# Performance work log

Measured on AMD Instinct MI355X. Metric: run time of the kernel, lower is better.

The kernel has to match this reference:

```python
import jax, jax.numpy as jnp
import numpy as np

SR = 44100.0
J, Q = 12, 16
W0 = 2.0 * np.pi      # MorletWavelet.freq_to_w_at_s(1.0, s=1.0) -> w = 2*pi*f*s
N_SIG = 3.0           # wavelet support = +/- N_SIG standard deviations


def _make_wavelet_bank():
    """Morlet filter bank: J octaves, Q steps/octave, highest freq = nyquist.
    Returns centered, zero-padded real/imag filter stacks of shape (K, Lmax)."""
    dt = 1.0 / SR
    nyq = SR / 2.0
    wavelets = []
    for j in range(J):
        for q in range(Q):
            f = nyq / (2.0 ** (j + q / Q))
            s = 1.0 / f                      # center freq f = W0/(2*pi*s) = 1/s
            M = int(np.ceil(N_SIG * s * SR))  # half support in samples
            t = np.arange(-M, M + 1) * dt
            psi = (np.pi ** -0.25) / np.sqrt(s) \
                * np.exp(1j * W0 * t / s) * np.exp(-0.5 * (t / s) ** 2)
            psi = psi / np.sum(np.abs(psi))   # L1 normalization
            wavelets.append(psi.astype(np.complex64))
    Lmax = max(len(p) for p in wavelets)       # odd (2*M_max + 1)
    bank = np.zeros((len(wavelets), Lmax), np.complex64)
    for i, p in enumerate(wavelets):
        left = (Lmax - len(p)) // 2            # center-pad each wavelet
        bank[i, left:left + len(p)] = p
    return bank


def setup_inputs() -> dict:
    key = jax.random.key(0)
    x = jax.random.normal(key, (2, 1, 32768), dtype=jnp.float32)
    bank = _make_wavelet_bank()
    return {
        "x": x,
        "filt_real": jnp.asarray(bank.real, dtype=jnp.float32),
        "filt_imag": jnp.asarray(bank.imag, dtype=jnp.float32),
    }


def _scat1d(x, filt_real, filt_imag):
    # x: (B, 1, T); filters: (K, L) with L odd. Equivalent to the torch path:
    # pad input by L//2, cross-correlate (F.conv1d) with each complex wavelet,
    # take the modulus. Done via FFT (same math, efficient for ~47k-tap kernels).
    K, L = filt_real.shape
    B, C, T = x.shape  # C == 1 (squeeze_channels=True)
    P = L // 2
    xp = jnp.pad(x[:, 0, :], ((0, 0), (P, P)))       # (B, T + 2P)
    n_full = xp.shape[-1] + L - 1
    N = 1 << (n_full - 1).bit_length()               # next pow2 FFT size
    X = jnp.fft.rfft(xp, N)                          # (B, N//2+1)
    Gr = jnp.fft.rfft(filt_real[:, ::-1], N)         # flip -> corr via conv
    Gi = jnp.fft.rfft(filt_imag[:, ::-1], N)         # (K, N//2+1)
    lo = L - 1                                       # valid-corr offset
    yr = jnp.fft.irfft(X[:, None, :] * Gr[None], N)[..., lo:lo + T]
    yi = jnp.fft.irfft(X[:, None, :] * Gi[None], N)[..., lo:lo + T]
    return jnp.sqrt(yr * yr + yi * yi)               # (B, K, T) modulus


def reference(x, filt_real, filt_imag):
    return _scat1d(x, filt_real, filt_imag)
```

## Files before the change

kernel.cpp:

```cpp
#include <hip/hip_runtime.h>
#include <math.h>

#define T_LEN   32768
#define NK      192
#define NB      2
#define KDIR    48
#define MAXM    56

struct SParams {
  int m1e[144];
  int slot[144];
  int voff[144];
  int ab[9];
  int jb[11];
};

__device__ __forceinline__ int j2_of_q(int q) {
  return 4 + (q >= 5) + (q >= 10) + (q >= 15);
}

__global__ __launch_bounds__(256) void k_pre(float* __restrict__ ws, SParams P,
                                             int zbase, int zn) {
  int tid = threadIdx.x;
  if (blockIdx.y == 144) {
    int stride = gridDim.x * 256;
    for (int i = blockIdx.x * 256 + tid; i < zn; i += stride) ws[zbase + i] = 0.f;
    return;
  }
  int ki = blockIdx.y;
  int slotc = P.slot[ki];
  int M1e = P.m1e[ki];
  float* dst = ws + P.voff[ki];
  int nent = 2 * M1e + 2;
  int k = ki + 48;
  int j = k >> 4, q = k & 15;
  float sig = 2.f * exp2f((float)(16 * j + q) * 0.0625f);
  float s1 = sig * 0.86602540378f;
  float gc = -0.5f / (s1 * s1);
  float om = 6.28318530718f / sig;
  float norm = 1.f / (2.50662827463f * s1 * erff((float)M1e / (1.41421356237f * s1)));
  #pragma unroll
  for (int e0 = 0; e0 < 4; ++e0) {
    int e = blockIdx.x * 1024 + e0 * 256 + tid;
    if (e >= slotc) continue;
    if (e >= nent) { dst[2 * e] = 0.f; dst[2 * e + 1] = 0.f; continue; }
    float mm = (float)(e - M1e);
    float g = __expf(gc * mm * mm) * norm;
    float sn, cs; __sincosf(om * mm, &sn, &cs);
    dst[2 * e] = g * cs;
    dst[2 * e + 1] = g * sn;
  }
}


template<int J, int G, int S, int CH>
__device__ __forceinline__ void deep_path(const float* __restrict__ x,
                                          float* __restrict__ ws, const SParams& P,
                                          int q, int rc, int tid,
                                          float* xs, float* red) {
  constexpr int d = 1 << J;
  constexpr int E = 2048;
  const int tile = rc / CH;
  const int chunk = rc % CH;
  const int ki = 16 * (J - 3) + q;
  const int J2 = j2_of_q(q);
  const int slot = P.slot[ki];
  const int e_base = chunk * (S * E);
  if (e_base >= slot) return;
  const int M1e = P.m1e[ki];
  const float* vt = ws + P.voff[ki];
  const int n0 = tile * G;
  const int ubase0 = (n0 - J2) * d - M1e;
  const float* xb0 = x;
  const float* xb1 = x + T_LEN;

  float acc[4 * G];
  #pragma unroll
  for (int i = 0; i < 4 * G; ++i) acc[i] = 0.f;

  #pragma unroll
  for (int s = 0; s < S; ++s) {
    int e0 = e_base + s * E;
    if (e0 >= slot) break;
    int Ech = slot - e0; if (Ech > E) Ech = E;
    int ub = ubase0 + e0;
    int Wn = Ech + (G - 1) * d + 2;
    if (ub < T_LEN && ub + Wn > 0) {
      int Wh = (Wn + 1) >> 1;
      for (int i = tid; i < Wh; i += 256) {
        int u0 = ub + 2 * i;
        bool ok = (unsigned)u0 <= (unsigned)(T_LEN - 2);
        int uc = ok ? u0 : 0;
        float2 a = *(const float2*)(xb0 + uc);
        float2 b = *(const float2*)(xb1 + uc);
        float4 w;
        w.x = ok ? a.x : 0.f; w.y = ok ? b.x : 0.f;
        w.z = ok ? a.y : 0.f; w.w = ok ? b.y : 0.f;
        *(float4*)(xs + 4 * i) = w;
      }
      __syncthreads();
      int pend = Ech >> 9;
      const float4* xp0 = (const float4*)xs + tid;
      const float* vte = vt + 2 * e0 + 4 * tid;
      float4 vp = *(const float4*)(vte);
      for (int ps = 0; ps < pend; ++ps) {
        float4 v = vp;
        if (ps + 1 < pend) vp = *(const float4*)(vte + ((ps + 1) << 10));
        const float4* xp = xp0 + (ps << 8);
        #pragma unroll
        for (int g = 0; g < G; ++g) {
          float4 xv = xp[g * (d >> 1)];
          acc[4 * g + 0] += v.x * xv.x + v.z * xv.z;
          acc[4 * g + 1] += v.y * xv.x + v.w * xv.z;
          acc[4 * g + 2] += v.x * xv.y + v.z * xv.w;
          acc[4 * g + 3] += v.y * xv.y + v.w * xv.w;
        }
      }
      __syncthreads();
    }
  }

  #pragma unroll
  for (int st = 1; st < 64; st <<= 1) {
    #pragma unroll
    for (int i = 0; i < 4 * G; ++i) acc[i] += __shfl_xor(acc[i], st, 64);
  }
  int wv = tid >> 6;
  if ((tid & 63) == 0) {
    #pragma unroll
    for (int gg = 0; gg < G; ++gg)
      *(float4*)(red + wv * 64 + 4 * gg) =
        make_float4(acc[4 * gg], acc[4 * gg + 1], acc[4 * gg + 2], acc[4 * gg + 3]);
  }
  __syncthreads();
  if (tid < 4 * G)
    red[256 + tid] = red[tid] + red[64 + tid] + red[128 + tid] + red[192 + tid];
  __syncthreads();
  if (tid < G) {
    int nidx = n0 + tid;
    int Ncu = (32767 >> J) + 17;
    if (nidx < Ncu) {
      float ar0 = red[256 + 4 * tid], ai0 = red[256 + 4 * tid + 1];
      float ar1 = red[256 + 4 * tid + 2], ai1 = red[256 + 4 * tid + 3];
      float ndf = (float)((nidx - J2) * d);
      float rev = ndf * exp2f(-(float)(16 * (J + 1) + q) * 0.0625f);
      rev -= floorf(rev);
      float sn, cs; __sincosf(rev * 6.28318530718f, &sn, &cs);
      float* ap = ws + P.ab[J - 3] + (q * 2) * Ncu * 2;
      float r0 = ar0 * cs - ai0 * sn, i0 = ar0 * sn + ai0 * cs;
      float r1 = ar1 * cs - ai1 * sn, i1 = ar1 * sn + ai1 * cs;
      if (CH == 1) {
        *(float2*)(ap + 2 * nidx) = make_float2(r0, i0);
        *(float2*)(ap + 2 * (Ncu + nidx)) = make_float2(r1, i1);
      } else {
        atomicAdd(ap + 2 * nidx, r0);
        atomicAdd(ap + 2 * nidx + 1, i0);
        atomicAdd(ap + 2 * (Ncu + nidx), r1);
        atomicAdd(ap + 2 * (Ncu + nidx) + 1, i1);
      }
    }
  }
}

template<int J, int TOUT, int LT>
__device__ __forceinline__ void small_path(const float* __restrict__ x,
                                           float* __restrict__ ws, const SParams& P,
                                           int q, int tile, int tid,
                                           float* xs, float* red) {
  constexpr int d = 1 << J;
  constexpr int TASKS = TOUT * 2;
  constexpr int SPLIT = 256 / TASKS;
  const int ki = 16 * (J - 3) + q;
  const int J2 = j2_of_q(q);
  const int M1e = P.m1e[ki];
  const int nent = 2 * M1e + 2;
  const float* vt = ws + P.voff[ki];
  const int Ncu = (32767 >> J) + 17;
  const int o0 = tile * TOUT;
  const int ub = (o0 - J2) * d - M1e;
  const int W = (TOUT - 1) * d + nent;
  const int PS = W + (((W - 1) >> J) << 1) + 4;
  const float* xb0 = x;
  const float* xb1 = x + T_LEN;
  for (int i = tid; i < W; i += 256) {
    int u = ub + i;
    bool ok = (unsigned)u < (unsigned)T_LEN;
    int uc = ok ? u : 0;
    float a = xb0[uc]; a = ok ? a : 0.f;
    float bv = xb1[uc]; bv = ok ? bv : 0.f;
    int ad = i + ((i >> J) << 1);
    xs[ad] = a; xs[PS + ad] = bv;
  }
  __syncthreads();
  int o = tid & (TOUT - 1);
  int b = (tid >> LT) & 1;
  int seg = tid >> (LT + 1);
  int per = ((nent >> 1) + SPLIT - 1) / SPLIT;
  int e_lo = 2 * per * seg; if (e_lo > nent) e_lo = nent;
  int e_hi = e_lo + 2 * per; if (e_hi > nent) e_hi = nent;
  const float* pl = xs + b * PS;
  int sb = o * d;
  float ar = 0.f, ai = 0.f;
  #pragma unroll 4
  for (int e = e_lo; e < e_hi; e += 2) {
    float4 v = *(const float4*)(vt + 2 * e);
    int s = sb + e;
    float2 xv = *(const float2*)(pl + s + ((s >> J) << 1));
    ar += v.x * xv.x + v.z * xv.y;
    ai += v.y * xv.x + v.w * xv.y;
  }
  if (SPLIT > 1) {
    red[tid] = ar; red[256 + tid] = ai;
    __syncthreads();
    if (seg == 0) {
      #pragma unroll
      for (int ss = 1; ss < SPLIT; ++ss) {
        ar += red[tid + ss * TASKS];
        ai += red[256 + tid + ss * TASKS];
      }
    }
  }
  if (seg == 0 && o0 + o < Ncu) {
    int nidx = o0 + o;
    float ndf = (float)((nidx - J2) * d);
    float rev = ndf * exp2f(-(float)(16 * (J + 1) + q) * 0.0625f);
    rev -= floorf(rev);
    float sn, cs; __sincosf(rev * 6.28318530718f, &sn, &cs);
    float* ap = ws + P.ab[J - 3] + (q * 2) * Ncu * 2;
    *(float2*)(ap + 2 * (b * Ncu + nidx)) = make_float2(ar * cs - ai * sn, ar * sn + ai * cs);
  }
}

__device__ __forceinline__ void direct_path(const float* __restrict__ x,
                                            const float* __restrict__ fr,
                                            const float* __restrict__ fi,
                                            float* __restrict__ out, int Lmax,
                                            int rem, int tid,
                                            float* xs, float* red) {
  int b = rem / 1536;
  int r2 = rem - b * 1536;
  int k = r2 >> 5;
  int t0 = (r2 & 31) << 10;
  int j = k >> 4, q = k & 15;
  int M = (int)ceil(6.0 * exp2((double)j + (double)q * 0.0625)) + 2;
  int P = Lmax >> 1;
  float* frs = red;
  float* fis = red + 128;
  int xlen = 1024 + 2 * M;
  const float* xb = x + b * T_LEN;
  for (int i = tid; i < xlen; i += 256) {
    int u = t0 - M + i;
    xs[i] = (u >= 0 && u < T_LEN) ? xb[u] : 0.f;
  }
  if (tid < 4) xs[xlen + tid] = 0.f;
  const float* frk = fr + (size_t)k * Lmax + (P - M);
  const float* fik = fi + (size_t)k * Lmax + (P - M);
  int tl = 2 * M + 1;
  for (int i = tid; i < tl; i += 256) { frs[i] = frk[i]; fis[i] = fik[i]; }
  if (tid < 3) { frs[tl + tid] = 0.f; fis[tl + tid] = 0.f; }
  __syncthreads();
  float ar0 = 0.f, ar1 = 0.f, ar2 = 0.f, ar3 = 0.f;
  float ai0 = 0.f, ai1 = 0.f, ai2 = 0.f, ai3 = 0.f;
  const float4* xsv = (const float4*)(xs + 4 * tid);
  float4 w0 = xsv[0];
  int groups = (tl + 3) >> 2;
  for (int g = 0; g < groups; ++g) {
    float4 w1 = xsv[g + 1];
    float4 f4 = *(const float4*)(frs + 4 * g);
    float4 h4 = *(const float4*)(fis + 4 * g);
    ar0 += f4.x * w0.x + f4.y * w0.y + f4.z * w0.z + f4.w * w0.w;
    ai0 += h4.x * w0.x + h4.y * w0.y + h4.z * w0.z + h4.w * w0.w;
    ar1 += f4.x * w0.y + f4.y * w0.z + f4.z * w0.w + f4.w * w1.x;
    ai1 += h4.x * w0.y + h4.y * w0.z + h4.z * w0.w + h4.w * w1.x;
    ar2 += f4.x * w0.z + f4.y * w0.w + f4.z * w1.x + f4.w * w1.y;
    ai2 += h4.x * w0.z + h4.y * w0.w + h4.z * w1.x + h4.w * w1.y;
    ar3 += f4.x * w0.w + f4.y * w1.x + f4.z * w1.y + f4.w * w1.z;
    ai3 += h4.x * w0.w + h4.y * w1.x + h4.z * w1.y + h4.w * w1.z;
    w0 = w1;
  }
  size_t ob = (size_t)(b * NK + k) * T_LEN + t0 + 4 * tid;
  float4 res;
  res.x = sqrtf(ar0 * ar0 + ai0 * ai0);
  res.y = sqrtf(ar1 * ar1 + ai1 * ai1);
  res.z = sqrtf(ar2 * ar2 + ai2 * ai2);
  res.w = sqrtf(ar3 * ar3 + ai3 * ai3);
  *(float4*)(out + ob) = res;
}

__global__ __launch_bounds__(256) void k_s1(const float* __restrict__ x,
                                            const float* __restrict__ fr,
                                            const float* __restrict__ fi,
                                            float* __restrict__ out, int Lmax,
                                            float* __restrict__ ws, SParams P) {
  __shared__ __align__(16) float xs[8200];
  __shared__ __align__(16) float red[512];
  int bx = blockIdx.x, tid = threadIdx.x;
  int o = 0;
  #pragma unroll
  for (int t = 1; t < 10; ++t) if (bx >= P.jb[t]) o = t;
  int rem = bx - P.jb[o];
  if (o == 9) { direct_path(x, fr, fi, out, Lmax, rem, tid, xs, red); return; }
  int j = 11 - o;
  int rc = rem >> 4, q = rem & 15;
  switch (j) {
    case 11: deep_path<11, 2, 3, 8>(x, ws, P, q, rc, tid, xs, red); break;
    case 10: deep_path<10, 3, 3, 4>(x, ws, P, q, rc, tid, xs, red); break;
    case 9:  deep_path<9, 4, 3, 2>(x, ws, P, q, rc, tid, xs, red); break;
    case 8:  deep_path<8, 8, 3, 1>(x, ws, P, q, rc, tid, xs, red); break;
    case 7:  deep_path<7, 16, 2, 1>(x, ws, P, q, rc, tid, xs, red); break;
    case 6:  small_path<6, 32, 5>(x, ws, P, q, rc, tid, xs, red); break;
    case 5:  small_path<5, 64, 6>(x, ws, P, q, rc, tid, xs, red); break;
    case 4:  small_path<4, 128, 7>(x, ws, P, q, rc, tid, xs, red); break;
    default: small_path<3, 128, 7>(x, ws, P, q, rc, tid, xs, red); break;
  }
}

__global__ __launch_bounds__(256) void k_stage2(const float* __restrict__ ws,
                                                float* __restrict__ out, SParams P) {
  __shared__ __align__(16) float sA[2][8][48][2];
  int by = blockIdx.y;
  int bx = blockIdx.x, tid = threadIdx.x;
  int k0 = KDIR + 2 * by;
  int j = k0 >> 4;
  int d = 1 << j;
  int Ncu = (32767 >> j) + 17;
  int nbb = (bx << 8) >> j;
  int sstep = 8192 >> j;
  #pragma unroll
  for (int kk = 0; kk < 2; ++kk) {
    int q = (k0 + kk) & 15;
    int ntap = 2 * j2_of_q(q) + 1;
    const float* A0 = ws + P.ab[j - 3] + (q * 2) * Ncu * 2;
    int Ci = (255 >> j) + ntap + 1;
    #pragma unroll
    for (int pi = 0; pi < 8; ++pi) {
      int i = pi & 3, p = pi >> 2;
      const float* Ap = A0 + p * Ncu * 2 + 2 * (nbb + i * sstep);
      for (int c = tid; c < Ci; c += 256)
        *(float2*)(&sA[kk][pi][c][0]) = *(const float2*)(Ap + 2 * c);
    }
  }
  __syncthreads();
  int t0 = (bx << 8) + tid;
  int phi = t0 & (d - 1);
  int nl = (t0 >> j) - nbb;
  float fd = (float)d;
  #pragma unroll
  for (int kk = 0; kk < 2; ++kk) {
    int k = k0 + kk, q = k & 15;
    int J2 = j2_of_q(q);
    int ntap = 2 * J2 + 1;
    float sig = 2.f * exp2f((float)(16 * j + q) * 0.0625f);
    float s2 = sig * 0.5f;
    float inv2 = 1.f / (s2 * s2);
    float u0 = (float)(phi + J2 * d);
    float eg = __expf(-0.5f * u0 * u0 * inv2);
    float mf = __expf((fd * u0 - 0.5f * fd * fd) * inv2);
    float qf = __expf(-fd * fd * inv2);
    float Z = 0.f;
    float sr0 = 0.f, si0 = 0.f, sr1 = 0.f, si1 = 0.f;
    float sr2 = 0.f, si2 = 0.f, sr3 = 0.f, si3 = 0.f;
    float tr0 = 0.f, ti0 = 0.f, tr1 = 0.f, ti1 = 0.f;
    float tr2 = 0.f, ti2 = 0.f, tr3 = 0.f, ti3 = 0.f;
    const float* base = &sA[kk][0][nl][0];
    for (int rr = 0; rr < ntap; ++rr) {
      float w = eg; eg *= mf; mf *= qf; Z += w;
      float2 a0 = *(const float2*)(base + (0 * 48 + rr) * 2);
      float2 a1 = *(const float2*)(base + (1 * 48 + rr) * 2);
      float2 a2 = *(const float2*)(base + (2 * 48 + rr) * 2);
      float2 a3 = *(const float2*)(base + (3 * 48 + rr) * 2);
      float2 b0 = *(const float2*)(base + (4 * 48 + rr) * 2);
      float2 b1 = *(const float2*)(base + (5 * 48 + rr) * 2);
      float2 b2 = *(const float2*)(base + (6 * 48 + rr) * 2);
      float2 b3 = *(const float2*)(base + (7 * 48 + rr) * 2);
      sr0 += w * a0.x; si0 += w * a0.y; sr1 += w * a1.x; si1 += w * a1.y;
      sr2 += w * a2.x; si2 += w * a2.y; sr3 += w * a3.x; si3 += w * a3.y;
      tr0 += w * b0.x; ti0 += w * b0.y; tr1 += w * b1.x; ti1 += w * b1.y;
      tr2 += w * b2.x; ti2 += w * b2.y; tr3 += w * b3.x; ti3 += w * b3.y;
    }
    float zi = 1.f / Z;
    size_t ob0 = (size_t)k * T_LEN + t0;
    size_t ob1 = (size_t)(NK + k) * T_LEN + t0;
    out[ob0]         = sqrtf(sr0 * sr0 + si0 * si0) * zi;
    out[ob0 + 8192]  = sqrtf(sr1 * sr1 + si1 * si1) * zi;
    out[ob0 + 16384] = sqrtf(sr2 * sr2 + si2 * si2) * zi;
    out[ob0 + 24576] = sqrtf(sr3 * sr3 + si3 * si3) * zi;
    out[ob1]         = sqrtf(tr0 * tr0 + ti0 * ti0) * zi;
    out[ob1 + 8192]  = sqrtf(tr1 * tr1 + ti1 * ti1) * zi;
    out[ob1 + 16384] = sqrtf(tr2 * tr2 + ti2 * ti2) * zi;
    out[ob1 + 24576] = sqrtf(tr3 * tr3 + ti3 * ti3) * zi;
  }
}

extern "C" void kernel_launch(void* const* d_in, const int* in_sizes, int n_in,
                              void* d_out, int out_size, void* d_ws, size_t ws_size,
                              hipStream_t stream) {
  const float* x  = (const float*)d_in[0];
  const float* fr = (const float*)d_in[1];
  const float* fi = (const float*)d_in[2];
  float* out = (float*)d_out;
  float* ws  = (float*)d_ws;
  int Lmax = in_sizes[1] / NK;

  SParams Pm;
  int cur = 0, maxslot = 0;
  for (int ki = 0; ki < 144; ++ki) {
    int j = (ki + 48) >> 4, q = ki & 15;
    double sig = 2.0 * exp2(((double)(16 * j + q)) / 16.0);
    double s1 = sig * 0.86602540378443864676;
    int M1 = (int)ceil(3.5 * s1);
    int M1e = (M1 + 1) & ~1;
    int slotc = (2 * M1e + 2 + 511) & ~511;
    Pm.m1e[ki] = M1e;
    Pm.slot[ki] = slotc;
    Pm.voff[ki] = cur;
    cur += 2 * slotc;
    if (slotc > maxslot) maxslot = slotc;
  }
  for (int j = 3; j <= 11; ++j) {
    Pm.ab[j - 3] = cur;
    cur += 32 * ((32767 >> j) + 17) * 2;
  }
  const int DG[5]  = {2, 3, 4, 8, 16};
  const int DCH[5] = {8, 4, 2, 1, 1};
  const int STO[4] = {32, 64, 128, 128};
  Pm.jb[0] = 0;
  for (int o = 0; o < 9; ++o) {
    int j = 11 - o;
    int Ncu = (32767 >> j) + 17;
    int cnt;
    if (o < 5) {
      int tiles = (Ncu + DG[o] - 1) / DG[o];
      cnt = tiles * DCH[o] * 16;
    } else {
      int TOUT = STO[o - 5];
      cnt = ((Ncu + TOUT - 1) / TOUT) * 16;
    }
    Pm.jb[o + 1] = Pm.jb[o] + cnt;
  }
  Pm.jb[10] = Pm.jb[9] + (T_LEN / 1024) * KDIR * NB;

  int zbase = Pm.ab[6];
  int zn = (Pm.ab[8] + 32 * ((32767 >> 11) + 17) * 2) - zbase;

  k_pre<<<dim3((maxslot + 1023) / 1024, 145), dim3(256), 0, stream>>>(ws, Pm, zbase, zn);
  k_s1<<<dim3(Pm.jb[10]), dim3(256), 0, stream>>>(x, fr, fi, out, Lmax, ws, Pm);
  k_stage2<<<dim3(T_LEN / (256 * 4), (NK - KDIR) / 2), dim3(256), 0, stream>>>(ws, out, Pm);
}
```

Before: 229.9 us.

## Add register-only path for deepest octaves and retune tile sizes

Adds a reg_path for octaves 11 and 10. It reads input samples straight from global memory into registers, without staging them in LDS, and splits the wavelet taps across chunks that merge their results through atomics. The deep_path tap chunk size E is made a template parameter and lowered, and the small_path output tile sizes are halved for octaves 4 to 6. Shared memory drops accordingly, which aims to raise occupancy and spread work over more blocks. The cost is more global traffic in the register path and more blocks and atomics overall.

```diff
diff --git a/kernel.cpp b/kernel.cpp
--- a/kernel.cpp
+++ b/kernel.cpp
@@ -53,13 +53,111 @@
 }
 
 
-template<int J, int G, int S, int CH>
+template<int J, int G, int CH>
+__device__ __forceinline__ void reg_path(const float* __restrict__ x,
+                                         float* __restrict__ ws, const SParams& P,
+                                         int q, int rc, int tid, float* red) {
+  constexpr int d = 1 << J;
+  const int tile = rc / CH;
+  const int chunk = rc % CH;
+  const int ki = 16 * (J - 3) + q;
+  const int J2 = j2_of_q(q);
+  const int slot = P.slot[ki];
+  const int per = ((slot + CH - 1) / CH + 511) & ~511;
+  const int c0 = chunk * per;
+  if (c0 >= slot) return;
+  int c1 = c0 + per; if (c1 > slot) c1 = slot;
+  const int M1e = P.m1e[ki];
+  const float* vt = ws + P.voff[ki];
+  const int n0 = tile * G;
+  const int ub0 = (n0 - J2) * d - M1e + c0;
+  const float* xb0 = x;
+  const float* xb1 = x + T_LEN;
+
+  float acc[4 * G];
+  #pragma unroll
+  for (int i = 0; i < 4 * G; ++i) acc[i] = 0.f;
+
+  int npass = (c1 - c0) >> 9;
+  const float* vte = vt + 2 * c0 + 4 * tid;
+  const int hi_lim = T_LEN - 512 - (G - 1) * d;
+  float4 vp = *(const float4*)vte;
+  for (int p = 0; p < npass; ++p) {
+    float4 v = vp;
+    if (p + 1 < npass) vp = *(const float4*)(vte + ((p + 1) << 10));
+    int ub = ub0 + (p << 9);
+    int u = ub + 2 * tid;
+    if (ub >= 0 && ub <= hi_lim) {
+      #pragma unroll
+      for (int g = 0; g < G; ++g) {
+        float2 a = *(const float2*)(xb0 + u + g * d);
+        float2 b = *(const float2*)(xb1 + u + g * d);
+        acc[4 * g + 0] += v.x * a.x + v.z * a.y;
+        acc[4 * g + 1] += v.y * a.x + v.w * a.y;
+        acc[4 * g + 2] += v.x * b.x + v.z * b.y;
+        acc[4 * g + 3] += v.y * b.x + v.w * b.y;
+      }
+    } else if (ub < T_LEN && ub + 512 + (G - 1) * d > 0) {
+      #pragma unroll
+      for (int g = 0; g < G; ++g) {
+        int ug = u + g * d;
+        int uc = min(max(ug, 0), T_LEN - 2);
+        float2 a = *(const float2*)(xb0 + uc);
+        float2 b = *(const float2*)(xb1 + uc);
+        bool ok = (unsigned)ug <= (unsigned)(T_LEN - 2);
+        float ax = ok ? a.x : 0.f, ay = ok ? a.y : 0.f;
+        float bx = ok ? b.x : 0.f, by = ok ? b.y : 0.f;
+        acc[4 * g + 0] += v.x * ax + v.z * ay;
+        acc[4 * g + 1] += v.y * ax + v.w * ay;
+        acc[4 * g + 2] += v.x * bx + v.z * by;
+        acc[4 * g + 3] += v.y * bx + v.w * by;
+      }
+    }
+  }
+
+  #pragma unroll
+  for (int st = 1; st < 64; st <<= 1) {
+    #pragma unroll
+    for (int i = 0; i < 4 * G; ++i) acc[i] += __shfl_xor(acc[i], st, 64);
+  }
+  int wv = tid >> 6;
+  if ((tid & 63) == 0) {
+    #pragma unroll
+    for (int gg = 0; gg < G; ++gg)
+      *(float4*)(red + wv * 64 + 4 * gg) =
+        make_float4(acc[4 * gg], acc[4 * gg + 1], acc[4 * gg + 2], acc[4 * gg + 3]);
+  }
+  __syncthreads();
+  if (tid < 4 * G)
+    red[256 + tid] = red[tid] + red[64 + tid] + red[128 + tid] + red[192 + tid];
+  __syncthreads();
+  if (tid < G) {
+    int nidx = n0 + tid;
+    int Ncu = (32767 >> J) + 17;
+    if (nidx < Ncu) {
+      float ar0 = red[256 + 4 * tid], ai0 = red[256 + 4 * tid + 1];
+      float ar1 = red[256 + 4 * tid + 2], ai1 = red[256 + 4 * tid + 3];
+      float ndf = (float)((nidx - J2) * d);
+      float rev = ndf * exp2f(-(float)(16 * (J + 1) + q) * 0.0625f);
+      rev -= floorf(rev);
+      float sn, cs; __sincosf(rev * 6.28318530718f, &sn, &cs);
+      float* ap = ws + P.ab[J - 3] + (q * 2) * Ncu * 2;
+      float r0 = ar0 * cs - ai0 * sn, i0 = ar0 * sn + ai0 * cs;
+      float r1 = ar1 * cs - ai1 * sn, i1 = ar1 * sn + ai1 * cs;
+      atomicAdd(ap + 2 * nidx, r0);
+      atomicAdd(ap + 2 * nidx + 1, i0);
+      atomicAdd(ap + 2 * (Ncu + nidx), r1);
+      atomicAdd(ap + 2 * (Ncu + nidx) + 1, i1);
+    }
+  }
+}
+
+template<int J, int G, int S, int CH, int E>
 __device__ __forceinline__ void deep_path(const float* __restrict__ x,
                                           float* __restrict__ ws, const SParams& P,
                                           int q, int rc, int tid,
                                           float* xs, float* red) {
   constexpr int d = 1 << J;
-  constexpr int E = 2048;
   const int tile = rc / CH;
   const int chunk = rc % CH;
   const int ki = 16 * (J - 3) + q;
@@ -292,7 +390,7 @@
                                             const float* __restrict__ fi,
                                             float* __restrict__ out, int Lmax,
                                             float* __restrict__ ws, SParams P) {
-  __shared__ __align__(16) float xs[8200];
+  __shared__ __align__(16) float xs[6920];
   __shared__ __align__(16) float red[512];
   int bx = blockIdx.x, tid = threadIdx.x;
   int o = 0;
@@ -303,14 +401,14 @@
   int j = 11 - o;
   int rc = rem >> 4, q = rem & 15;
   switch (j) {
-    case 11: deep_path<11, 2, 3, 8>(x, ws, P, q, rc, tid, xs, red); break;
-    case 10: deep_path<10, 3, 3, 4>(x, ws, P, q, rc, tid, xs, red); break;
-    case 9:  deep_path<9, 4, 3, 2>(x, ws, P, q, rc, tid, xs, red); break;
-    case 8:  deep_path<8, 8, 3, 1>(x, ws, P, q, rc, tid, xs, red); break;
-    case 7:  deep_path<7, 16, 2, 1>(x, ws, P, q, rc, tid, xs, red); break;
-    case 6:  small_path<6, 32, 5>(x, ws, P, q, rc, tid, xs, red); break;
-    case 5:  small_path<5, 64, 6>(x, ws, P, q, rc, tid, xs, red); break;
-    case 4:  small_path<4, 128, 7>(x, ws, P, q, rc, tid, xs, red); break;
+    case 11: reg_path<11, 2, 8>(x, ws, P, q, rc, tid, red); break;
+    case 10: reg_path<10, 3, 4>(x, ws, P, q, rc, tid, red); break;
+    case 9:  deep_path<9, 4, 4, 2, 1536>(x, ws, P, q, rc, tid, xs, red); break;
+    case 8:  deep_path<8, 8, 4, 1, 1536>(x, ws, P, q, rc, tid, xs, red); break;
+    case 7:  deep_path<7, 16, 2, 1, 1536>(x, ws, P, q, rc, tid, xs, red); break;
+    case 6:  small_path<6, 16, 4>(x, ws, P, q, rc, tid, xs, red); break;
+    case 5:  small_path<5, 32, 5>(x, ws, P, q, rc, tid, xs, red); break;
+    case 4:  small_path<4, 64, 6>(x, ws, P, q, rc, tid, xs, red); break;
     default: small_path<3, 128, 7>(x, ws, P, q, rc, tid, xs, red); break;
   }
 }
@@ -423,7 +521,7 @@
   }
   const int DG[5]  = {2, 3, 4, 8, 16};
   const int DCH[5] = {8, 4, 2, 1, 1};
-  const int STO[4] = {32, 64, 128, 128};
+  const int STO[4] = {16, 32, 64, 128};
   Pm.jb[0] = 0;
   for (int o = 0; o < 9; ++o) {
     int j = 11 - o;
```

New measurement: 227.4 us. No clear change (-1.1%).

## Stream deep-octave correlation from a zero-padded input in registers

Applied to the files above, without the earlier changes.

A pre-pass now writes a zero-padded copy of both input batches into the workspace, so every path can read the signal without bounds checks. The shared-memory-staged deep path is replaced by a register path that reads the padded input and filter taps straight from global memory. It uses double-buffered loads, a fixed group of 4 outputs, and chunked reduction. The small-path tile sizes are reduced and shared memory halved with a launch-bounds occupancy hint of 8, trading more blocks and global cache traffic for fewer syncs and higher occupancy.

```diff
diff --git a/kernel.cpp b/kernel.cpp
--- a/kernel.cpp
+++ b/kernel.cpp
@@ -6,6 +6,9 @@
 #define NB      2
 #define KDIR    48
 #define MAXM    56
+#define PADL    40960
+#define PADR    40960
+#define XLEN    (PADL + T_LEN + PADR)
 
 struct SParams {
   int m1e[144];
@@ -13,15 +16,27 @@
   int voff[144];
   int ab[9];
   int jb[11];
+  int xoff;
 };
 
 __device__ __forceinline__ int j2_of_q(int q) {
   return 4 + (q >= 5) + (q >= 10) + (q >= 15);
 }
 
-__global__ __launch_bounds__(256) void k_pre(float* __restrict__ ws, SParams P,
+__global__ __launch_bounds__(256) void k_pre(const float* __restrict__ x,
+                                             float* __restrict__ ws, SParams P,
                                              int zbase, int zn) {
   int tid = threadIdx.x;
+  if (blockIdx.y == 145) {
+    int stride = gridDim.x * 256;
+    float* xp = ws + P.xoff;
+    for (int i = blockIdx.x * 256 + tid; i < 2 * XLEN; i += stride) {
+      int b = i >= XLEN;
+      int u = i - (b ? XLEN : 0) - PADL;
+      xp[i] = ((unsigned)u < (unsigned)T_LEN) ? x[b * T_LEN + u] : 0.f;
+    }
+    return;
+  }
   if (blockIdx.y == 144) {
     int stride = gridDim.x * 256;
     for (int i = blockIdx.x * 256 + tid; i < zn; i += stride) ws[zbase + i] = 0.f;
@@ -53,95 +68,102 @@
 }
 
 
-template<int J, int G, int S, int CH>
-__device__ __forceinline__ void deep_path(const float* __restrict__ x,
-                                          float* __restrict__ ws, const SParams& P,
-                                          int q, int rc, int tid,
-                                          float* xs, float* red) {
+template<int J, int CH>
+__device__ __forceinline__ void reg_path(const float* __restrict__ xpad,
+                                         float* __restrict__ ws, const SParams& P,
+                                         int q, int rc, int tid, float* red) {
   constexpr int d = 1 << J;
-  constexpr int E = 2048;
   const int tile = rc / CH;
   const int chunk = rc % CH;
   const int ki = 16 * (J - 3) + q;
   const int J2 = j2_of_q(q);
   const int slot = P.slot[ki];
-  const int e_base = chunk * (S * E);
-  if (e_base >= slot) return;
+  const int per = CH == 1 ? slot : (((slot + CH - 1) / CH + 511) & ~511);
+  const int c0 = chunk * per;
+  if (c0 >= slot) return;
+  int c1 = c0 + per; if (c1 > slot) c1 = slot;
   const int M1e = P.m1e[ki];
   const float* vt = ws + P.voff[ki];
-  const int n0 = tile * G;
-  const int ubase0 = (n0 - J2) * d - M1e;
-  const float* xb0 = x;
-  const float* xb1 = x + T_LEN;
-
-  float acc[4 * G];
-  #pragma unroll
-  for (int i = 0; i < 4 * G; ++i) acc[i] = 0.f;
-
-  #pragma unroll
-  for (int s = 0; s < S; ++s) {
-    int e0 = e_base + s * E;
-    if (e0 >= slot) break;
-    int Ech = slot - e0; if (Ech > E) Ech = E;
-    int ub = ubase0 + e0;
-    int Wn = Ech + (G - 1) * d + 2;
-    if (ub < T_LEN && ub + Wn > 0) {
-      int Wh = (Wn + 1) >> 1;
-      for (int i = tid; i < Wh; i += 256) {
-        int u0 = ub + 2 * i;
-        bool ok = (unsigned)u0 <= (unsigned)(T_LEN - 2);
-        int uc = ok ? u0 : 0;
-        float2 a = *(const float2*)(xb0 + uc);
-        float2 b = *(const float2*)(xb1 + uc);
-        float4 w;
-        w.x = ok ? a.x : 0.f; w.y = ok ? b.x : 0.f;
-        w.z = ok ? a.y : 0.f; w.w = ok ? b.y : 0.f;
-        *(float4*)(xs + 4 * i) = w;
-      }
-      __syncthreads();
-      int pend = Ech >> 9;
-      const float4* xp0 = (const float4*)xs + tid;
-      const float* vte = vt + 2 * e0 + 4 * tid;
-      float4 vp = *(const float4*)(vte);
-      for (int ps = 0; ps < pend; ++ps) {
-        float4 v = vp;
-        if (ps + 1 < pend) vp = *(const float4*)(vte + ((ps + 1) << 10));
-        const float4* xp = xp0 + (ps << 8);
-        #pragma unroll
-        for (int g = 0; g < G; ++g) {
-          float4 xv = xp[g * (d >> 1)];
-          acc[4 * g + 0] += v.x * xv.x + v.z * xv.z;
-          acc[4 * g + 1] += v.y * xv.x + v.w * xv.z;
-          acc[4 * g + 2] += v.x * xv.y + v.z * xv.w;
-          acc[4 * g + 3] += v.y * xv.y + v.w * xv.w;
-        }
-      }
-      __syncthreads();
-    }
-  }
+  const int n0 = tile * 4;
+  const int ub0 = (n0 - J2) * d - M1e + c0;
+  if (CH > 1 && (ub0 >= T_LEN || ub0 + (c1 - c0) + 3 * d <= 0)) return;
+  const float* xa  = xpad + PADL + ub0 + 2 * tid;
+  const float* xb2 = xa + XLEN;
+  const float* vte = vt + 2 * c0 + 4 * tid;
+  const int npass = (c1 - c0) >> 9;
+
+  float acc[16];
+  #pragma unroll
+  for (int i = 0; i < 16; ++i) acc[i] = 0.f;
+
+  float4 vA, vB;
+  float2 a0A, a1A, a2A, a3A, b0A, b1A, b2A, b3A;
+  float2 a0B, a1B, a2B, a3B, b0B, b1B, b2B, b3B;
+
+#define RLOAD(S_, pp) \
+  v##S_ = *(const float4*)(vte + ((pp) << 10)); \
+  a0##S_ = *(const float2*)(xa + ((pp) << 9)); \
+  a1##S_ = *(const float2*)(xa + ((pp) << 9) + d); \
+  a2##S_ = *(const float2*)(xa + ((pp) << 9) + 2 * d); \
+  a3##S_ = *(const float2*)(xa + ((pp) << 9) + 3 * d); \
+  b0##S_ = *(const float2*)(xb2 + ((pp) << 9)); \
+  b1##S_ = *(const float2*)(xb2 + ((pp) << 9) + d); \
+  b2##S_ = *(const float2*)(xb2 + ((pp) << 9) + 2 * d); \
+  b3##S_ = *(const float2*)(xb2 + ((pp) << 9) + 3 * d);
+
+#define RFMA(S_) \
+  acc[0]  += v##S_.x * a0##S_.x + v##S_.z * a0##S_.y; \
+  acc[1]  += v##S_.y * a0##S_.x + v##S_.w * a0##S_.y; \
+  acc[2]  += v##S_.x * b0##S_.x + v##S_.z * b0##S_.y; \
+  acc[3]  += v##S_.y * b0##S_.x + v##S_.w * b0##S_.y; \
+  acc[4]  += v##S_.x * a1##S_.x + v##S_.z * a1##S_.y; \
+  acc[5]  += v##S_.y * a1##S_.x + v##S_.w * a1##S_.y; \
+  acc[6]  += v##S_.x * b1##S_.x + v##S_.z * b1##S_.y; \
+  acc[7]  += v##S_.y * b1##S_.x + v##S_.w * b1##S_.y; \
+  acc[8]  += v##S_.x * a2##S_.x + v##S_.z * a2##S_.y; \
+  acc[9]  += v##S_.y * a2##S_.x + v##S_.w * a2##S_.y; \
+  acc[10] += v##S_.x * b2##S_.x + v##S_.z * b2##S_.y; \
+  acc[11] += v##S_.y * b2##S_.x + v##S_.w * b2##S_.y; \
+  acc[12] += v##S_.x * a3##S_.x + v##S_.z * a3##S_.y; \
+  acc[13] += v##S_.y * a3##S_.x + v##S_.w * a3##S_.y; \
+  acc[14] += v##S_.x * b3##S_.x + v##S_.z * b3##S_.y; \
+  acc[15] += v##S_.y * b3##S_.x + v##S_.w * b3##S_.y;
+
+  int p = 0;
+  RLOAD(A, 0)
+  while (p + 2 <= npass) {
+    RLOAD(B, p + 1)
+    RFMA(A)
+    if (p + 2 < npass) { RLOAD(A, p + 2) }
+    RFMA(B)
+    p += 2;
+  }
+  if (p < npass) { RFMA(A) }
+#undef RLOAD
+#undef RFMA
 
   #pragma unroll
   for (int st = 1; st < 64; st <<= 1) {
     #pragma unroll
-    for (int i = 0; i < 4 * G; ++i) acc[i] += __shfl_xor(acc[i], st, 64);
+    for (int i = 0; i < 16; ++i) acc[i] += __shfl_xor(acc[i], st, 64);
   }
   int wv = tid >> 6;
   if ((tid & 63) == 0) {
     #pragma unroll
-    for (int gg = 0; gg < G; ++gg)
-      *(float4*)(red + wv * 64 + 4 * gg) =
+    for (int gg = 0; gg < 4; ++gg)
+      *(float4*)(red + wv * 16 + 4 * gg) =
         make_float4(acc[4 * gg], acc[4 * gg + 1], acc[4 * gg + 2], acc[4 * gg + 3]);
   }
   __syncthreads();
-  if (tid < 4 * G)
-    red[256 + tid] = red[tid] + red[64 + tid] + red[128 + tid] + red[192 + tid];
+  if (tid < 16)
+    red[64 + tid] = red[tid] + red[16 + tid] + red[32 + tid] + red[48 + tid];
   __syncthreads();
-  if (tid < G) {
+  if (tid < 4) {
     int nidx = n0 + tid;
     int Ncu = (32767 >> J) + 17;
     if (nidx < Ncu) {
-      float ar0 = red[256 + 4 * tid], ai0 = red[256 + 4 * tid + 1];
-      float ar1 = red[256 + 4 * tid + 2], ai1 = red[256 + 4 * tid + 3];
+      float ar0 = red[64 + 4 * tid],     ai0 = red[64 + 4 * tid + 1];
+      float ar1 = red[64 + 4 * tid + 2], ai1 = red[64 + 4 * tid + 3];
       float ndf = (float)((nidx - J2) * d);
       float rev = ndf * exp2f(-(float)(16 * (J + 1) + q) * 0.0625f);
       rev -= floorf(rev);
@@ -163,7 +185,7 @@
 }
 
 template<int J, int TOUT, int LT>
-__device__ __forceinline__ void small_path(const float* __restrict__ x,
+__device__ __forceinline__ void small_path(const float* __restrict__ xpad,
                                            float* __restrict__ ws, const SParams& P,
                                            int q, int tile, int tid,
                                            float* xs, float* red) {
@@ -180,14 +202,10 @@
   const int ub = (o0 - J2) * d - M1e;
   const int W = (TOUT - 1) * d + nent;
   const int PS = W + (((W - 1) >> J) << 1) + 4;
-  const float* xb0 = x;
-  const float* xb1 = x + T_LEN;
+  const float* xa = xpad + PADL + ub;
   for (int i = tid; i < W; i += 256) {
-    int u = ub + i;
-    bool ok = (unsigned)u < (unsigned)T_LEN;
-    int uc = ok ? u : 0;
-    float a = xb0[uc]; a = ok ? a : 0.f;
-    float bv = xb1[uc]; bv = ok ? bv : 0.f;
+    float a = xa[i];
+    float bv = xa[XLEN + i];
     int ad = i + ((i >> J) << 1);
     xs[ad] = a; xs[PS + ad] = bv;
   }
@@ -231,7 +249,7 @@
   }
 }
 
-__device__ __forceinline__ void direct_path(const float* __restrict__ x,
+__device__ __forceinline__ void direct_path(const float* __restrict__ xpad,
                                             const float* __restrict__ fr,
                                             const float* __restrict__ fi,
                                             float* __restrict__ out, int Lmax,
@@ -247,11 +265,8 @@
   float* frs = red;
   float* fis = red + 128;
   int xlen = 1024 + 2 * M;
-  const float* xb = x + b * T_LEN;
-  for (int i = tid; i < xlen; i += 256) {
-    int u = t0 - M + i;
-    xs[i] = (u >= 0 && u < T_LEN) ? xb[u] : 0.f;
-  }
+  const float* xb = xpad + b * XLEN + PADL + t0 - M;
+  for (int i = tid; i < xlen; i += 256) xs[i] = xb[i];
   if (tid < 4) xs[xlen + tid] = 0.f;
   const float* frk = fr + (size_t)k * Lmax + (P - M);
   const float* fik = fi + (size_t)k * Lmax + (P - M);
@@ -287,31 +302,31 @@
   *(float4*)(out + ob) = res;
 }
 
-__global__ __launch_bounds__(256) void k_s1(const float* __restrict__ x,
-                                            const float* __restrict__ fr,
-                                            const float* __restrict__ fi,
-                                            float* __restrict__ out, int Lmax,
-                                            float* __restrict__ ws, SParams P) {
-  __shared__ __align__(16) float xs[8200];
+__global__ __launch_bounds__(256, 8) void k_s1(const float* __restrict__ fr,
+                                               const float* __restrict__ fi,
+                                               float* __restrict__ out, int Lmax,
+                                               float* __restrict__ ws, SParams P) {
+  __shared__ __align__(16) float xs[4100];
   __shared__ __align__(16) float red[512];
+  const float* xpad = ws + P.xoff;
   int bx = blockIdx.x, tid = threadIdx.x;
   int o = 0;
   #pragma unroll
   for (int t = 1; t < 10; ++t) if (bx >= P.jb[t]) o = t;
   int rem = bx - P.jb[o];
-  if (o == 9) { direct_path(x, fr, fi, out, Lmax, rem, tid, xs, red); return; }
+  if (o == 9) { direct_path(xpad, fr, fi, out, Lmax, rem, tid, xs, red); return; }
   int j = 11 - o;
   int rc = rem >> 4, q = rem & 15;
   switch (j) {
-    case 11: deep_path<11, 2, 3, 8>(x, ws, P, q, rc, tid, xs, red); break;
-    case 10: deep_path<10, 3, 3, 4>(x, ws, P, q, rc, tid, xs, red); break;
-    case 9:  deep_path<9, 4, 3, 2>(x, ws, P, q, rc, tid, xs, red); break;
-    case 8:  deep_path<8, 8, 3, 1>(x, ws, P, q, rc, tid, xs, red); break;
-    case 7:  deep_path<7, 16, 2, 1>(x, ws, P, q, rc, tid, xs, red); break;
-    case 6:  small_path<6, 32, 5>(x, ws, P, q, rc, tid, xs, red); break;
-    case 5:  small_path<5, 64, 6>(x, ws, P, q, rc, tid, xs, red); break;
-    case 4:  small_path<4, 128, 7>(x, ws, P, q, rc, tid, xs, red); break;
-    default: small_path<3, 128, 7>(x, ws, P, q, rc, tid, xs, red); break;
+    case 11: reg_path<11, 8>(xpad, ws, P, q, rc, tid, red); break;
+    case 10: reg_path<10, 4>(xpad, ws, P, q, rc, tid, red); break;
+    case 9:  reg_path<9, 2>(xpad, ws, P, q, rc, tid, red); break;
+    case 8:  reg_path<8, 1>(xpad, ws, P, q, rc, tid, red); break;
+    case 7:  reg_path<7, 1>(xpad, ws, P, q, rc, tid, red); break;
+    case 6:  small_path<6, 8, 3>(xpad, ws, P, q, rc, tid, xs, red); break;
+    case 5:  small_path<5, 16, 4>(xpad, ws, P, q, rc, tid, xs, red); break;
+    case 4:  small_path<4, 32, 5>(xpad, ws, P, q, rc, tid, xs, red); break;
+    default: small_path<3, 64, 6>(xpad, ws, P, q, rc, tid, xs, red); break;
   }
 }
 
@@ -421,17 +436,18 @@
     Pm.ab[j - 3] = cur;
     cur += 32 * ((32767 >> j) + 17) * 2;
   }
-  const int DG[5]  = {2, 3, 4, 8, 16};
+  Pm.xoff = cur;
+  cur += 2 * XLEN;
+
   const int DCH[5] = {8, 4, 2, 1, 1};
-  const int STO[4] = {32, 64, 128, 128};
+  const int STO[4] = {8, 16, 32, 64};
   Pm.jb[0] = 0;
   for (int o = 0; o < 9; ++o) {
     int j = 11 - o;
     int Ncu = (32767 >> j) + 17;
     int cnt;
     if (o < 5) {
-      int tiles = (Ncu + DG[o] - 1) / DG[o];
-      cnt = tiles * DCH[o] * 16;
+      cnt = (Ncu / 4) * DCH[o] * 16;
     } else {
       int TOUT = STO[o - 5];
       cnt = ((Ncu + TOUT - 1) / TOUT) * 16;
@@ -443,7 +459,7 @@
   int zbase = Pm.ab[6];
   int zn = (Pm.ab[8] + 32 * ((32767 >> 11) + 17) * 2) - zbase;
 
-  k_pre<<<dim3((maxslot + 1023) / 1024, 145), dim3(256), 0, stream>>>(ws, Pm, zbase, zn);
-  k_s1<<<dim3(Pm.jb[10]), dim3(256), 0, stream>>>(x, fr, fi, out, Lmax, ws, Pm);
+  k_pre<<<dim3((maxslot + 1023) / 1024, 146), dim3(256), 0, stream>>>(x, ws, Pm, zbase, zn);
+  k_s1<<<dim3(Pm.jb[10]), dim3(256), 0, stream>>>(fr, fi, out, Lmax, ws, Pm);
   k_stage2<<<dim3(T_LEN / (256 * 4), (NK - KDIR) / 2), dim3(256), 0, stream>>>(ws, out, Pm);
 }
```

New measurement: 316.2 us. 1.38x slower.
